# Performance work log

Measured on AMD Instinct MI355X. Metric: run time of the kernel, lower is better.

The kernel has to match this reference:

```python
import jax, jax.numpy as jnp
import numpy as np

MARGIN = 0.09
SCALE_POS = 2.0
SCALE_NEG = 40.0
EPS = 1e-05
THRESH1 = 0.501
THRESH2 = 0.531


def setup_inputs() -> dict:
    key = jax.random.key(0)
    k1, k2 = jax.random.split(key)
    B, D, N_CLASSES = 4096, 1024, 64
    feats = jax.random.normal(k1, (B, D), dtype=jnp.float32)
    # thresholds in the loss assume cosine-scale similarities -> L2 normalize
    feats = feats / jnp.linalg.norm(feats, axis=1, keepdims=True)
    labels = jax.random.randint(k2, (B,), 0, N_CLASSES, dtype=jnp.int64)
    return {"feats": feats, "labels": labels}


def reference(feats, labels):
    B = feats.shape[0]
    sim = jnp.matmul(feats, feats.T)  # [B, B]
    eq = labels[:, None] == labels[None, :]
    neg_mask = ~eq
    pos_mask = eq & (sim < 1.0 - EPS)  # drops self-similarity (~1)
    # per-row max over negatives; rows with no negatives -> -inf -> no pos survive
    max_neg = jnp.max(jnp.where(neg_mask, sim, -jnp.inf), axis=1)  # [B]
    pos_mask = pos_mask & ((sim - MARGIN) < max_neg[:, None])
    n_pos = jnp.sum(pos_mask, axis=1)
    n_neg = jnp.sum(neg_mask, axis=1)
    pos_sum = jnp.sum(jnp.where(pos_mask, jnp.exp(-SCALE_POS * sim), 0.0), axis=1)
    neg_sum = jnp.sum(jnp.where(neg_mask, jnp.exp(SCALE_NEG * sim), 0.0), axis=1)
    pos_loss = (1.0 / SCALE_POS) * jnp.log(
        (pos_sum + np.exp(-SCALE_POS * THRESH1)) / (n_pos + 1.0))
    neg_loss = (1.0 / SCALE_NEG) * jnp.log(
        (neg_sum + np.exp(SCALE_NEG * THRESH2)) / (n_neg + 1.0))
    per_row = jnp.log(5.33 + jnp.exp(pos_loss + neg_loss))  # [B]
    valid = (n_neg >= 1) & (n_pos >= 1)
    return jnp.sum(jnp.where(valid, per_row, 0.0)) / B
```

## Files before the change

### kernel.cpp

```cpp
#include <hip/hip_runtime.h>
#include <hip/hip_bf16.h>
#include <math.h>

typedef __attribute__((ext_vector_type(4))) float floatx4;

#define MARGIN_C    0.09f
#define ONE_M_EPS   0.99999f
#define NCLS        64
#define MEMSTRIDE   256

__device__ __forceinline__ unsigned short f2bf(float f) {
    unsigned u = __float_as_uint(f);
    u += 0x7fffu + ((u >> 16) & 1u);
    return (unsigned short)(u >> 16);
}
__device__ __forceinline__ float bf2f(unsigned short v) {
    return __uint_as_float(((unsigned)v) << 16);
}
__device__ __forceinline__ unsigned fkey(float f) {
    unsigned u = __float_as_uint(f);
    return (u >> 31) ? ~u : (u | 0x80000000u);
}
__device__ __forceinline__ float fdec(unsigned k) {
    return __uint_as_float((k >> 31) ? (k & 0x7fffffffu) : ~k);
}
__device__ __forceinline__ void gld16(const void* g, void* l) {
    __builtin_amdgcn_global_load_lds(
        (const __attribute__((address_space(1))) void*)g,
        (__attribute__((address_space(3))) void*)l, 16, 0, 0);
}

__global__ __launch_bounds__(256) void cvt_build(const float* __restrict__ in,
                                                 unsigned* __restrict__ out8,
                                                 float* __restrict__ statz,
                                                 const int* __restrict__ labels,
                                                 int* __restrict__ members,
                                                 int* __restrict__ classCount,
                                                 float* __restrict__ loss_out,
                                                 int n4, int nz4, int ncvt, int Bn) {
    __shared__ int cnt;
    const int bid = blockIdx.x;
    const int t = threadIdx.x;
    if (bid < ncvt) {
        int i = bid * 256 + t;
        if (bid == 0 && t == 0) loss_out[0] = 0.0f;
        if (i < nz4) ((float4*)statz)[i] = make_float4(0.f, 0.f, 0.f, 0.f);
        if (i >= n4) return;
        float4 v = ((const float4*)in)[i];
        int w = __builtin_amdgcn_cvt_pk_fp8_f32(v.x, v.y, 0, false);
        w = __builtin_amdgcn_cvt_pk_fp8_f32(v.z, v.w, w, true);
        out8[i] = (unsigned)w;
    } else {
        const int c = bid - ncvt;
        if (t == 0) cnt = 0;
        __syncthreads();
        for (int j = t; j < Bn; j += 256) {
            if (labels[j] == c) {
                int p = atomicAdd(&cnt, 1);
                if (p < MEMSTRIDE) members[c * MEMSTRIDE + p] = j;
            }
        }
        __syncthreads();
        if (t == 0) classCount[c] = (cnt < MEMSTRIDE) ? cnt : MEMSTRIDE;
    }
}

__global__ __launch_bounds__(256, 2) void gemm_fused(const unsigned char* __restrict__ fb8,
                                                     const int* __restrict__ labels,
                                                     float* __restrict__ negsum,
                                                     unsigned* __restrict__ negmax,
                                                     unsigned short* __restrict__ pairsim,
                                                     int Bn, int Dn) {
    __shared__ __align__(16) unsigned char As[2][8192];
    __shared__ __align__(16) unsigned char Bs[2][8192];
    __shared__ int Lrow[128], Lcol[128];

    const int bid = blockIdx.x;
    int by = (int)((sqrtf(8.f * (float)bid + 1.f) - 1.f) * 0.5f);
    while ((by + 1) * (by + 2) / 2 <= bid) by++;
    while (by * (by + 1) / 2 > bid) by--;
    const int bx = bid - by * (by + 1) / 2;
    const bool diag = (bx == by);

    const int t = threadIdx.x;
    const int wave = t >> 6, lane = t & 63;
    const int wr = wave >> 1, wc = wave & 1;
    const int quad = lane >> 4, m16 = lane & 15;

    if (t < 128) Lrow[t] = labels[by * 128 + t];
    else         Lcol[t - 128] = labels[bx * 128 + (t - 128)];

    const int r = t >> 2, a = t & 3;
    const int gofs = ((2 * a) ^ (r & 6)) * 8;
    const unsigned char* gA0 = fb8 + (size_t)(by * 128 + r) * Dn + gofs;
    const unsigned char* gB0 = fb8 + (size_t)(bx * 128 + r) * Dn + gofs;
    const unsigned char* gA1 = gA0 + (size_t)64 * Dn;
    const unsigned char* gB1 = gB0 + (size_t)64 * Dn;
    const int lb = t * 16;

    floatx4 acc[4][4];
#pragma unroll
    for (int i = 0; i < 4; i++)
#pragma unroll
        for (int j = 0; j < 4; j++) acc[i][j] = (floatx4){0.f, 0.f, 0.f, 0.f};

    const int fragA = (wr * 64 + m16) * 64;
    const int fragB = (wc * 64 + m16) * 64;
    const int sw = m16 & 6;
    const int sK0 = (quad ^ sw) * 8;
    const int sK1 = ((quad + 4) ^ sw) * 8;

    const int NS = Dn / 64;

    gld16(gA0, &As[0][lb]);
    gld16(gA1, &As[0][4096 + lb]);
    if (!diag) {
        gld16(gB0, &Bs[0][lb]);
        gld16(gB1, &Bs[0][4096 + lb]);
    }
    __syncthreads();

    for (int s = 0; s < NS; s++) {
        if (s + 1 < NS) {
            const int ko = (s + 1) * 64;
            const int nb = (s + 1) & 1;
            gld16(gA0 + ko, &As[nb][lb]);
            gld16(gA1 + ko, &As[nb][4096 + lb]);
            if (!diag) {
                gld16(gB0 + ko, &Bs[nb][lb]);
                gld16(gB1 + ko, &Bs[nb][4096 + lb]);
            }
        }
        __builtin_amdgcn_sched_barrier(0);

        const unsigned char* as_ = &As[s & 1][0];
        const unsigned char* bs_ = diag ? as_ : &Bs[s & 1][0];
        long af[4], bfr[4];
#pragma unroll
        for (int i = 0; i < 4; i++) af[i]  = *(const long*)(as_ + fragA + i * 1024 + sK0);
#pragma unroll
        for (int i = 0; i < 4; i++) bfr[i] = *(const long*)(bs_ + fragB + i * 1024 + sK0);
#pragma unroll
        for (int i = 0; i < 4; i++)
#pragma unroll
            for (int j = 0; j < 4; j++)
                acc[i][j] = __builtin_amdgcn_mfma_f32_16x16x32_fp8_fp8(af[i], bfr[j], acc[i][j], 0, 0, 0);
#pragma unroll
        for (int i = 0; i < 4; i++) af[i]  = *(const long*)(as_ + fragA + i * 1024 + sK1);
#pragma unroll
        for (int i = 0; i < 4; i++) bfr[i] = *(const long*)(bs_ + fragB + i * 1024 + sK1);
#pragma unroll
        for (int i = 0; i < 4; i++)
#pragma unroll
            for (int j = 0; j < 4; j++)
                acc[i][j] = __builtin_amdgcn_mfma_f32_16x16x32_fp8_fp8(af[i], bfr[j], acc[i][j], 0, 0, 0);

        __syncthreads();
    }

    const bool offd = !diag;
    int cl[4], gc[4];
#pragma unroll
    for (int j = 0; j < 4; j++) {
        cl[j] = Lcol[wc * 64 + j * 16 + m16];
        gc[j] = bx * 128 + wc * 64 + j * 16 + m16;
    }

    float nsm[4] = {0.f, 0.f, 0.f, 0.f};
    float nmm[4] = {-INFINITY, -INFINITY, -INFINITY, -INFINITY};

#pragma unroll
    for (int i = 0; i < 4; i++) {
#pragma unroll
        for (int rr = 0; rr < 4; rr++) {
            const int rowl = wr * 64 + i * 16 + quad * 4 + rr;
            const int rl = Lrow[rowl];
            const int gr = by * 128 + rowl;
            float ns = 0.f, nm = -INFINITY;
#pragma unroll
            for (int j = 0; j < 4; j++) {
                const float s = acc[i][j][rr];
                if (cl[j] != rl) {
                    const float e = __expf(40.f * s);
                    ns += e;
                    nm = fmaxf(nm, s);
                    nsm[j] += e;
                    nmm[j] = fmaxf(nmm[j], s);
                } else if ((gr != gc[j]) & (s < ONE_M_EPS)) {
                    const unsigned short v = f2bf(s);
                    pairsim[(size_t)gr * Bn + gc[j]] = v;
                    if (offd) pairsim[(size_t)gc[j] * Bn + gr] = v;
                }
            }
#pragma unroll
            for (int o = 8; o; o >>= 1) {
                ns += __shfl_down(ns, o, 64);
                nm = fmaxf(nm, __shfl_down(nm, o, 64));
            }
            if (m16 == 0) {
                atomicAdd(negsum + gr, ns);
                atomicMax(negmax + gr, fkey(nm));
            }
        }
    }
    if (offd) {
#pragma unroll
        for (int j = 0; j < 4; j++) {
            float v = nsm[j], m = nmm[j];
            v += __shfl_down(v, 16, 64);
            m = fmaxf(m, __shfl_down(m, 16, 64));
            v += __shfl_down(v, 32, 64);
            m = fmaxf(m, __shfl_down(m, 32, 64));
            if (quad == 0) {
                atomicAdd(negsum + gc[j], v);
                atomicMax(negmax + gc[j], fkey(m));
            }
        }
    }
}

__global__ __launch_bounds__(256) void pos_final(const unsigned short* __restrict__ pairsim,
                                                 const int* __restrict__ labels,
                                                 const int* __restrict__ members,
                                                 const int* __restrict__ classCount,
                                                 const unsigned* __restrict__ negmax,
                                                 const float* __restrict__ negsum,
                                                 float* __restrict__ out, int Bn) {
    __shared__ float part[4];
    const int t = threadIdx.x;
    const int wave = t >> 6, lane = t & 63;
    float wacc = 0.f;
#pragma unroll
    for (int rr = 0; rr < 4; rr++) {
        const int r = blockIdx.x * 16 + wave * 4 + rr;
        if (r >= Bn) break;
        const int lab = labels[r];
        const int n = classCount[lab];
        const int base = lab * MEMSTRIDE;
        const float mx = fdec(negmax[r]);
        const unsigned short* prow = pairsim + (size_t)r * Bn;

        float ps = 0.f, pc = 0.f;
        for (int j = lane; j < n; j += 64) {
            const int m = members[base + j];
            if (m != r) {
                const float s = bf2f(prow[m]);
                if ((s - MARGIN_C) < mx) {
                    ps += __expf(-2.f * s);
                    pc += 1.f;
                }
            }
        }
#pragma unroll
        for (int o = 32; o; o >>= 1) {
            ps += __shfl_down(ps, o, 64);
            pc += __shfl_down(pc, o, 64);
        }
        if (lane == 0) {
            const int nneg = Bn - n;
            if (nneg >= 1 && pc >= 0.5f) {
                float pl = 0.5f * logf((ps + expf(-2.f * 0.501f)) / (pc + 1.f));
                float nl = (1.f / 40.f) * logf((negsum[r] + expf(40.f * 0.531f)) / ((float)nneg + 1.f));
                wacc += logf(5.33f + expf(pl + nl));
            }
        }
    }
    if (lane == 0) part[wave] = wacc;
    __syncthreads();
    if (t == 0) {
        atomicAdd(out, (part[0] + part[1] + part[2] + part[3]) / (float)Bn);
    }
}

extern "C" void kernel_launch(void* const* d_in, const int* in_sizes, int n_in,
                              void* d_out, int out_size, void* d_ws, size_t ws_size,
                              hipStream_t stream) {
    const float* feats = (const float*)d_in[0];
    const int* labels  = (const int*)d_in[1];
    float* out = (float*)d_out;

    const int Bn = in_sizes[1];
    const int Dn = in_sizes[0] / Bn;

    unsigned char* fb8 = (unsigned char*)d_ws;
    float* stats    = (float*)(fb8 + (size_t)Bn * Dn);
    float* negsum   = stats;
    unsigned* negmax = (unsigned*)(stats + Bn);
    int* classCount = (int*)(stats + 2 * Bn);
    int* members    = classCount + NCLS;
    unsigned short* pairsim = (unsigned short*)(members + NCLS * MEMSTRIDE);

    const int n4   = (Bn * Dn) / 4;
    const int nz4  = (2 * Bn) / 4;
    const int ncvt = (n4 + 255) / 256;
    cvt_build<<<ncvt + NCLS, 256, 0, stream>>>(feats, (unsigned*)fb8, stats, labels,
                                               members, classCount, out,
                                               n4, nz4, ncvt, Bn);

    const int nt = Bn / 128;
    const int ntri = nt * (nt + 1) / 2;
    gemm_fused<<<ntri, 256, 0, stream>>>(fb8, labels, negsum, negmax, pairsim, Bn, Dn);

    pos_final<<<(Bn + 15) / 16, 256, 0, stream>>>(pairsim, labels, members, classCount,
                                                  negmax, negsum, out, Bn);
}
```

Before: 113.6 us.

## Use 128x64 lower-triangular tiles with mirroring to drop diagonal-block special case

Replaces the 128x128 triangular tile grid with 128x64 tiles covering the lower triangle at 64-column granularity. Each wave now owns a 32x64 sub-tile, so the accumulator count halves and launch bounds rise to 4 blocks per SM for more occupancy. Off-diagonal tiles mirror their results, and diagonal 64-wide tiles are computed directly without the shared A/B special case. This doubles the block count, lowers the B reuse per tile and adds more atomics, in exchange for better load balance and latency hiding.

```diff
diff --git a/kernel.cpp b/kernel.cpp
--- a/kernel.cpp
+++ b/kernel.cpp
@@ -65,47 +65,46 @@
     }
 }
 
-__global__ __launch_bounds__(256, 2) void gemm_fused(const unsigned char* __restrict__ fb8,
+__global__ __launch_bounds__(256, 4) void gemm_fused(const unsigned char* __restrict__ fb8,
                                                      const int* __restrict__ labels,
                                                      float* __restrict__ negsum,
                                                      unsigned* __restrict__ negmax,
                                                      unsigned short* __restrict__ pairsim,
                                                      int Bn, int Dn) {
     __shared__ __align__(16) unsigned char As[2][8192];
-    __shared__ __align__(16) unsigned char Bs[2][8192];
-    __shared__ int Lrow[128], Lcol[128];
+    __shared__ __align__(16) unsigned char Bs[2][4096];
+    __shared__ int Lrow[128], Lcol[64];
 
     const int bid = blockIdx.x;
-    int by = (int)((sqrtf(8.f * (float)bid + 1.f) - 1.f) * 0.5f);
-    while ((by + 1) * (by + 2) / 2 <= bid) by++;
-    while (by * (by + 1) / 2 > bid) by--;
-    const int bx = bid - by * (by + 1) / 2;
-    const bool diag = (bx == by);
+    int by = (int)(sqrtf((float)bid + 0.25f) - 0.5f);
+    while ((by + 1) * (by + 2) <= bid) by++;
+    while (by * (by + 1) > bid) by--;
+    const int c64 = bid - by * (by + 1);
+    const int gcb = c64 * 64;
+    const bool mirror = (gcb < by * 128);
 
     const int t = threadIdx.x;
     const int wave = t >> 6, lane = t & 63;
-    const int wr = wave >> 1, wc = wave & 1;
     const int quad = lane >> 4, m16 = lane & 15;
 
     if (t < 128) Lrow[t] = labels[by * 128 + t];
-    else         Lcol[t - 128] = labels[bx * 128 + (t - 128)];
+    else if (t < 192) Lcol[t - 128] = labels[gcb + (t - 128)];
 
     const int r = t >> 2, a = t & 3;
     const int gofs = ((2 * a) ^ (r & 6)) * 8;
     const unsigned char* gA0 = fb8 + (size_t)(by * 128 + r) * Dn + gofs;
-    const unsigned char* gB0 = fb8 + (size_t)(bx * 128 + r) * Dn + gofs;
     const unsigned char* gA1 = gA0 + (size_t)64 * Dn;
-    const unsigned char* gB1 = gB0 + (size_t)64 * Dn;
+    const unsigned char* gB0 = fb8 + (size_t)(gcb + r) * Dn + gofs;
     const int lb = t * 16;
 
-    floatx4 acc[4][4];
-#pragma unroll
-    for (int i = 0; i < 4; i++)
+    floatx4 acc[2][4];
+#pragma unroll
+    for (int i = 0; i < 2; i++)
 #pragma unroll
         for (int j = 0; j < 4; j++) acc[i][j] = (floatx4){0.f, 0.f, 0.f, 0.f};
 
-    const int fragA = (wr * 64 + m16) * 64;
-    const int fragB = (wc * 64 + m16) * 64;
+    const int fragA = (wave * 32 + m16) * 64;
+    const int fragB = m16 * 64;
     const int sw = m16 & 6;
     const int sK0 = (quad ^ sw) * 8;
     const int sK1 = ((quad + 4) ^ sw) * 8;
@@ -114,10 +113,7 @@
 
     gld16(gA0, &As[0][lb]);
     gld16(gA1, &As[0][4096 + lb]);
-    if (!diag) {
-        gld16(gB0, &Bs[0][lb]);
-        gld16(gB1, &Bs[0][4096 + lb]);
-    }
+    gld16(gB0, &Bs[0][lb]);
     __syncthreads();
 
     for (int s = 0; s < NS; s++) {
@@ -126,31 +122,28 @@
             const int nb = (s + 1) & 1;
             gld16(gA0 + ko, &As[nb][lb]);
             gld16(gA1 + ko, &As[nb][4096 + lb]);
-            if (!diag) {
-                gld16(gB0 + ko, &Bs[nb][lb]);
-                gld16(gB1 + ko, &Bs[nb][4096 + lb]);
-            }
+            gld16(gB0 + ko, &Bs[nb][lb]);
         }
         __builtin_amdgcn_sched_barrier(0);
 
         const unsigned char* as_ = &As[s & 1][0];
-        const unsigned char* bs_ = diag ? as_ : &Bs[s & 1][0];
-        long af[4], bfr[4];
-#pragma unroll
-        for (int i = 0; i < 4; i++) af[i]  = *(const long*)(as_ + fragA + i * 1024 + sK0);
-#pragma unroll
-        for (int i = 0; i < 4; i++) bfr[i] = *(const long*)(bs_ + fragB + i * 1024 + sK0);
-#pragma unroll
-        for (int i = 0; i < 4; i++)
+        const unsigned char* bs_ = &Bs[s & 1][0];
+        long af[2], bfr[4];
+#pragma unroll
+        for (int i = 0; i < 2; i++) af[i]  = *(const long*)(as_ + fragA + i * 1024 + sK0);
+#pragma unroll
+        for (int j = 0; j < 4; j++) bfr[j] = *(const long*)(bs_ + fragB + j * 1024 + sK0);
+#pragma unroll
+        for (int i = 0; i < 2; i++)
 #pragma unroll
             for (int j = 0; j < 4; j++)
                 acc[i][j] = __builtin_amdgcn_mfma_f32_16x16x32_fp8_fp8(af[i], bfr[j], acc[i][j], 0, 0, 0);
 #pragma unroll
-        for (int i = 0; i < 4; i++) af[i]  = *(const long*)(as_ + fragA + i * 1024 + sK1);
-#pragma unroll
-        for (int i = 0; i < 4; i++) bfr[i] = *(const long*)(bs_ + fragB + i * 1024 + sK1);
-#pragma unroll
-        for (int i = 0; i < 4; i++)
+        for (int i = 0; i < 2; i++) af[i]  = *(const long*)(as_ + fragA + i * 1024 + sK1);
+#pragma unroll
+        for (int j = 0; j < 4; j++) bfr[j] = *(const long*)(bs_ + fragB + j * 1024 + sK1);
+#pragma unroll
+        for (int i = 0; i < 2; i++)
 #pragma unroll
             for (int j = 0; j < 4; j++)
                 acc[i][j] = __builtin_amdgcn_mfma_f32_16x16x32_fp8_fp8(af[i], bfr[j], acc[i][j], 0, 0, 0);
@@ -158,22 +151,21 @@
         __syncthreads();
     }
 
-    const bool offd = !diag;
     int cl[4], gc[4];
 #pragma unroll
     for (int j = 0; j < 4; j++) {
-        cl[j] = Lcol[wc * 64 + j * 16 + m16];
-        gc[j] = bx * 128 + wc * 64 + j * 16 + m16;
+        cl[j] = Lcol[j * 16 + m16];
+        gc[j] = gcb + j * 16 + m16;
     }
 
     float nsm[4] = {0.f, 0.f, 0.f, 0.f};
     float nmm[4] = {-INFINITY, -INFINITY, -INFINITY, -INFINITY};
 
 #pragma unroll
-    for (int i = 0; i < 4; i++) {
+    for (int i = 0; i < 2; i++) {
 #pragma unroll
         for (int rr = 0; rr < 4; rr++) {
-            const int rowl = wr * 64 + i * 16 + quad * 4 + rr;
+            const int rowl = wave * 32 + i * 16 + quad * 4 + rr;
             const int rl = Lrow[rowl];
             const int gr = by * 128 + rowl;
             float ns = 0.f, nm = -INFINITY;
@@ -189,7 +181,7 @@
                 } else if ((gr != gc[j]) & (s < ONE_M_EPS)) {
                     const unsigned short v = f2bf(s);
                     pairsim[(size_t)gr * Bn + gc[j]] = v;
-                    if (offd) pairsim[(size_t)gc[j] * Bn + gr] = v;
+                    if (mirror) pairsim[(size_t)gc[j] * Bn + gr] = v;
                 }
             }
 #pragma unroll
@@ -203,7 +195,7 @@
             }
         }
     }
-    if (offd) {
+    if (mirror) {
 #pragma unroll
         for (int j = 0; j < 4; j++) {
             float v = nsm[j], m = nmm[j];
@@ -298,8 +290,8 @@
                                                n4, nz4, ncvt, Bn);
 
     const int nt = Bn / 128;
-    const int ntri = nt * (nt + 1) / 2;
-    gemm_fused<<<ntri, 256, 0, stream>>>(fb8, labels, negsum, negmax, pairsim, Bn, Dn);
+    const int ngrid = nt * (nt + 1);
+    gemm_fused<<<ngrid, 256, 0, stream>>>(fb8, labels, negsum, negmax, pairsim, Bn, Dn);
 
     pos_final<<<(Bn + 15) / 16, 256, 0, stream>>>(pairsim, labels, members, classCount,
                                                   negmax, negsum, out, Bn);
```

Result: faster. 107.9 us (-5.0%).
